# Optimization experiments

Measured on AMD Instinct MI355X. Metric: run time of the kernel, lower is better.

## Reference

```python
import jax, jax.numpy as jnp
import numpy as np

FRAMES, PATCHES, DIM, HEADS, DFF, K = 256, 64, 512, 8, 1024, 128


def _mhsa(x, Wqkv, Wo, h):
    # standard multi-head self-attention, no bias, no norm (as in the repo)
    b, t, d = x.shape
    dh = d // h
    qkv = x @ Wqkv                                   # [b, t, 3d]
    q, k, v = jnp.split(qkv, 3, axis=-1)
    rs = lambda z: z.reshape(b, t, h, dh).transpose(0, 2, 1, 3)  # [b,h,t,dh]
    q, k, v = rs(q), rs(k), rs(v)
    att = jax.nn.softmax(jnp.einsum('bhqd,bhkd->bhqk', q, k) * (dh ** -0.5), axis=-1)
    out = jnp.einsum('bhqk,bhkd->bhqd', att, v)
    return out.transpose(0, 2, 1, 3).reshape(b, t, d) @ Wo


def _linformer(x, Wqkv, Wo, E, h):
    # Linformer: project K and V along the token axis with E before attention
    b, t, d = x.shape
    dh = d // h
    qkv = x @ Wqkv
    q, k, v = jnp.split(qkv, 3, axis=-1)
    rs = lambda z: z.reshape(b, t, h, dh).transpose(0, 2, 1, 3)
    q, k, v = rs(q), rs(k), rs(v)
    k = jnp.einsum('bhjd,jk->bhkd', k, E)            # [b,h,K,dh]
    v = jnp.einsum('bhjd,jk->bhkd', v, E)
    att = jax.nn.softmax(jnp.einsum('bhqd,bhkd->bhqk', q, k) * (dh ** -0.5), axis=-1)
    out = jnp.einsum('bhqk,bhkd->bhqd', att, v)
    return out.transpose(0, 2, 1, 3).reshape(b, t, d) @ Wo


def setup_inputs() -> dict:
    key = jax.random.key(0)
    ks = jax.random.split(key, 10)
    s = 0.02
    n = 1 + FRAMES * PATCHES
    return {
        'x': jax.random.normal(ks[0], (1, n, DIM), jnp.float32),
        'Wqkv_t': jax.random.normal(ks[1], (DIM, 3 * DIM), jnp.float32) * s,
        'Wo_t': jax.random.normal(ks[2], (DIM, DIM), jnp.float32) * s,
        'Wqkv_s': jax.random.normal(ks[3], (DIM, 3 * DIM), jnp.float32) * s,
        'Wo_s': jax.random.normal(ks[4], (DIM, DIM), jnp.float32) * s,
        'E': jax.random.normal(ks[5], (PATCHES + 1, K), jnp.float32) * s,
        'W1': jax.random.normal(ks[6], (DIM, DFF), jnp.float32) * s,
        'b1': jnp.zeros((DFF,), jnp.float32),
        'W2': jax.random.normal(ks[7], (DFF, DIM), jnp.float32) * s,
        'b2': jnp.zeros((DIM,), jnp.float32),
    }


def reference(x, Wqkv_t, Wo_t, Wqkv_s, Wo_s, E, W1, b1, W2, b2):
    b, n, d = x.shape
    f, p = FRAMES, PATCHES
    # split cls token
    cls, xt = x[:, :1], x[:, 1:]                      # [b,1,d], [b,f*p,d]
    # rearrange 'b (f p) d -> (b p) f d'
    xt = xt.reshape(b, f, p, d).transpose(0, 2, 1, 3).reshape(b * p, f, d)
    cls_t = jnp.tile(cls, (b * p // b, 1, 1))          # expand cls to batch b*p
    xt = jnp.concatenate([cls_t, xt], axis=1)          # [b*p, f+1, d]
    y = _mhsa(xt, Wqkv_t, Wo_t, HEADS) + xt            # time attention + residual
    cls2, y = y[:, :1], y[:, 1:]                       # [b*p,1,d], [b*p,f,d]
    # rearrange '(b p) f d -> (b f) p d'
    y = y.reshape(b, p, f, d).transpose(0, 2, 1, 3).reshape(b * f, p, d)
    cls_s = jnp.tile(cls2, (b * f // (b * p), 1, 1))   # expand cls to batch b*f
    y = jnp.concatenate([cls_s, y], axis=1)            # [b*f, p+1, d]
    y = _linformer(y, Wqkv_s, Wo_s, E, HEADS) + y      # space attention + residual
    # rearrange '(b f) p d -> b (f p) d' (token count is p+1 here, per source)
    y = y.reshape(b, f * (p + 1), d)
    h = jax.nn.gelu(y @ W1 + b1, approximate=False)    # nn.GELU is exact erf
    y = (h @ W2 + b2) + y                              # MLP + residual (dropout=eval)
    return y
```

## Files before the change

### kernel.cpp

```cpp
#include <hip/hip_runtime.h>


typedef unsigned short u16;
typedef unsigned int   u32;
typedef __attribute__((ext_vector_type(8))) short s16x8;
typedef __attribute__((ext_vector_type(4))) float f32x4;

__device__ __forceinline__ float b2f(u16 u) {
    return __uint_as_float(((u32)u) << 16);
}
__device__ __forceinline__ u16 f2b(float f) {
    u32 v = __float_as_uint(f);
    return (u16)((v + 0x7FFFu + ((v >> 16) & 1u)) >> 16);
}

__global__ __launch_bounds__(128) void build_xt_k(const float* __restrict__ x,
                                                  u16* __restrict__ xt) {
    int row = blockIdx.x;
    int p = row / 257, t = row % 257;
    long src = (t == 0) ? 0L : (long)(1 + (t - 1) * 64 + p);
    float4 v = ((const float4*)(x + src * 512))[threadIdx.x];
    ushort4 o;
    o.x = f2b(v.x); o.y = f2b(v.y); o.z = f2b(v.z); o.w = f2b(v.w);
    ((ushort4*)(xt + (long)row * 512))[threadIdx.x] = o;
}

__global__ __launch_bounds__(128) void build_ys_k(const u16* __restrict__ yt,
                                                  u16* __restrict__ ys) {
    int row = blockIdx.x;
    int f = row / 65, s = row % 65;
    long src = (s == 0) ? (long)((f & 63) * 257) : (long)((s - 1) * 257 + 1 + f);
    const uint2* sp = (const uint2*)(yt + src * 512);
    ((uint2*)(ys + (long)row * 512))[threadIdx.x] = sp[threadIdx.x];
}

__global__ __launch_bounds__(256) void store_f32(const u16* __restrict__ src,
                                                 float* __restrict__ dst) {
    long i = ((long)blockIdx.x * 256 + threadIdx.x) * 8;
    uint4 v = *(const uint4*)(src + i);
    float4 a, b;
    a.x = b2f((u16)v.x); a.y = b2f((u16)(v.x >> 16));
    a.z = b2f((u16)v.y); a.w = b2f((u16)(v.y >> 16));
    b.x = b2f((u16)v.z); b.y = b2f((u16)(v.z >> 16));
    b.z = b2f((u16)v.w); b.w = b2f((u16)(v.w >> 16));
    *(float4*)(dst + i) = a;
    *(float4*)(dst + i + 4) = b;
}

__global__ __launch_bounds__(256) void prep_wt(const float* __restrict__ src,
                                               u16* __restrict__ dst,
                                               int K, int N) {
    __shared__ float T[64][65];
    int k0 = blockIdx.x * 64, n0 = blockIdx.y * 64;
    int t = threadIdx.x;
    int r = t >> 2, q = t & 3;
#pragma unroll
    for (int i = 0; i < 4; ++i) {
        float4 v = *(const float4*)(src + (long)(k0 + r) * N + n0 + q * 16 + i * 4);
        T[r][q * 16 + i * 4 + 0] = v.x;
        T[r][q * 16 + i * 4 + 1] = v.y;
        T[r][q * 16 + i * 4 + 2] = v.z;
        T[r][q * 16 + i * 4 + 3] = v.w;
    }
    __syncthreads();
    u32 buf[8];
#pragma unroll
    for (int i = 0; i < 8; ++i) {
        float lo = T[q * 16 + 2 * i][r];
        float hi = T[q * 16 + 2 * i + 1][r];
        buf[i] = (u32)f2b(lo) | ((u32)f2b(hi) << 16);
    }
    u32* dp = (u32*)(dst + (long)(n0 + r) * K + k0 + q * 16);
#pragma unroll
    for (int i = 0; i < 8; ++i) dp[i] = buf[i];
}

template <int EPI, int OD>
__global__ __launch_bounds__(256) void gemm_mt(const u16* __restrict__ A, int lda,
                                               const u16* __restrict__ WT, int ldwt,
                                               int koff, int coff,
                                               const float* __restrict__ bias, int coff_b,
                                               const u16* __restrict__ res,
                                               void* __restrict__ outv,
                                               int Kd, int ldo) {
    __shared__ __align__(16) u16 As2[4][64][8];
    __shared__ __align__(16) u16 Bs2[4][256][8];
    const int tid = threadIdx.x;
    const int lane = tid & 63, w = tid >> 6;
    const int l15 = lane & 15, kg = lane >> 4;
    const int bn0 = blockIdx.x * 256, bm0 = blockIdx.y * 64;

    f32x4 acc[4][4];
#pragma unroll
    for (int i = 0; i < 4; ++i)
#pragma unroll
        for (int j = 0; j < 4; ++j) acc[i][j] = (f32x4){0.f, 0.f, 0.f, 0.f};

    const u16* Abase = A + (long)(bm0 + (tid >> 2)) * lda + (tid & 3) * 8;
    const u16* Bbase = WT + (long)(coff + bn0 + (tid >> 2)) * ldwt + koff + (tid & 3) * 8;
    const long bstep = (long)64 * ldwt;

    uint4 av  = *(const uint4*)(Abase);
    uint4 bv0 = *(const uint4*)(Bbase);
    uint4 bv1 = *(const uint4*)(Bbase + bstep);
    uint4 bv2 = *(const uint4*)(Bbase + 2 * bstep);
    uint4 bv3 = *(const uint4*)(Bbase + 3 * bstep);

    for (int kt = 0; kt < Kd; kt += 32) {
        __syncthreads();
        *(uint4*)&As2[tid & 3][tid >> 2][0] = av;
        *(uint4*)&Bs2[tid & 3][(tid >> 2) + 0][0]   = bv0;
        *(uint4*)&Bs2[tid & 3][(tid >> 2) + 64][0]  = bv1;
        *(uint4*)&Bs2[tid & 3][(tid >> 2) + 128][0] = bv2;
        *(uint4*)&Bs2[tid & 3][(tid >> 2) + 192][0] = bv3;
        int ktn = (kt + 32 < Kd) ? (kt + 32) : kt;
        av  = *(const uint4*)(Abase + ktn);
        bv0 = *(const uint4*)(Bbase + ktn);
        bv1 = *(const uint4*)(Bbase + ktn + bstep);
        bv2 = *(const uint4*)(Bbase + ktn + 2 * bstep);
        bv3 = *(const uint4*)(Bbase + ktn + 3 * bstep);
        __syncthreads();
        s16x8 af[4], bfr[4];
#pragma unroll
        for (int mf = 0; mf < 4; ++mf)
            af[mf] = *(const s16x8*)&As2[kg][mf * 16 + l15][0];
#pragma unroll
        for (int nf = 0; nf < 4; ++nf)
            bfr[nf] = *(const s16x8*)&Bs2[kg][w * 64 + nf * 16 + l15][0];
#pragma unroll
        for (int mf = 0; mf < 4; ++mf)
#pragma unroll
            for (int nf = 0; nf < 4; ++nf)
                acc[mf][nf] = __builtin_amdgcn_mfma_f32_16x16x32_bf16(
                    af[mf], bfr[nf], acc[mf][nf], 0, 0, 0);
    }

#pragma unroll
    for (int mf = 0; mf < 4; ++mf) {
#pragma unroll
        for (int nf = 0; nf < 4; ++nf) {
            int col = bn0 + w * 64 + nf * 16 + l15;
#pragma unroll
            for (int r = 0; r < 4; ++r) {
                int row = bm0 + mf * 16 + kg * 4 + r;
                float v = acc[mf][nf][r];
                if (EPI == 2 || EPI == 3) v += bias[coff_b + col];
                if (EPI == 2) v = 0.5f * v * (1.f + erff(v * 0.70710678118f));
                if (EPI == 1 || EPI == 3) v += b2f(res[(long)row * ldo + col]);
                if (OD == 0) ((u16*)outv)[(long)row * ldo + col] = f2b(v);
                else         ((float*)outv)[(long)row * ldo + col] = v;
            }
        }
    }
}

template <int EPI, int OD>
__global__ __launch_bounds__(256) void gemm_k(const u16* __restrict__ A, int lda,
                                              const float* __restrict__ W, int ldw,
                                              int koff, int coff,
                                              const float* __restrict__ bias, int coff_b,
                                              const u16* __restrict__ res,
                                              void* __restrict__ outv,
                                              int M, int N, int Kd, int ldo) {
    __shared__ float As[16][64];
    __shared__ float Ws[16][128];
    int tid = threadIdx.x;
    int tx = tid & 15, ty = tid >> 4;
    int bn0 = blockIdx.x * 128, bm0 = blockIdx.y * 64;

    float acc[4][8];
#pragma unroll
    for (int i = 0; i < 4; ++i)
#pragma unroll
        for (int j = 0; j < 8; ++j) acc[i][j] = 0.f;

    int am = tid >> 2, ak = (tid & 3) * 4;
    int wk = tid >> 4, wn = (tid & 15) * 8;
    const u16* Aptr = A + (long)(bm0 + am) * lda + ak;

    for (int kt = 0; kt < Kd; kt += 16) {
        const u32* ap = (const u32*)(Aptr + kt);
        u32 a0 = ap[0], a1 = ap[1];
        const float* wp = W + (long)(koff + kt + wk) * ldw + coff + bn0 + wn;
        float4 w0 = ((const float4*)wp)[0];
        float4 w1 = ((const float4*)wp)[1];
        __syncthreads();
        As[ak + 0][am] = b2f((u16)a0);
        As[ak + 1][am] = b2f((u16)(a0 >> 16));
        As[ak + 2][am] = b2f((u16)a1);
        As[ak + 3][am] = b2f((u16)(a1 >> 16));
        Ws[wk][wn + 0] = w0.x; Ws[wk][wn + 1] = w0.y;
        Ws[wk][wn + 2] = w0.z; Ws[wk][wn + 3] = w0.w;
        Ws[wk][wn + 4] = w1.x; Ws[wk][wn + 5] = w1.y;
        Ws[wk][wn + 6] = w1.z; Ws[wk][wn + 7] = w1.w;
        __syncthreads();
#pragma unroll
        for (int kk = 0; kk < 16; ++kk) {
            float a[4], b[8];
#pragma unroll
            for (int i = 0; i < 4; ++i) a[i] = As[kk][ty + 16 * i];
#pragma unroll
            for (int j = 0; j < 8; ++j) b[j] = Ws[kk][tx + 16 * j];
#pragma unroll
            for (int i = 0; i < 4; ++i)
#pragma unroll
                for (int j = 0; j < 8; ++j) acc[i][j] += a[i] * b[j];
        }
    }

#pragma unroll
    for (int i = 0; i < 4; ++i) {
        int row = bm0 + ty + 16 * i;
#pragma unroll
        for (int j = 0; j < 8; ++j) {
            int col = bn0 + tx + 16 * j;
            float v = acc[i][j];
            if (EPI == 2 || EPI == 3) v += bias[coff_b + col];
            if (EPI == 2) v = 0.5f * v * (1.f + erff(v * 0.70710678118f));
            if (EPI == 1 || EPI == 3) v += b2f(res[(long)row * ldo + col]);
            if (OD == 0) ((u16*)outv)[(long)row * ldo + col] = f2b(v);
            else         ((float*)outv)[(long)row * ldo + col] = v;
        }
    }
}

__global__ __launch_bounds__(256) void attn_t3(u16* __restrict__ QO,
                                               const u16* __restrict__ Kg,
                                               const u16* __restrict__ Vg,
                                               int hbase, int qbase) {
    __shared__ __align__(16) u16 sm[17280];
    const int tid = threadIdx.x;
    const int lane = tid & 63, w = tid >> 6;
    const int l15 = lane & 15, kg = lane >> 4;
    const int seq = blockIdx.x >> 2, hq = blockIdx.x & 3, h = hbase + hq;
    const int qc = blockIdx.y;
    const long row0 = (long)seq * 257;
    const int qcol = qbase + hq * 64;
    const int rb = qc * 128 + w * 32;

    u16* Kb = sm;
    u16* Vb = sm + 4224;
    u16* Pw = sm + 8320 + w * 2240;

    const u32* Ku = (const u32*)Kg;
    const u32* Vu = (const u32*)Vg;

    s16x8 qf[2][2];
#pragma unroll
    for (int mf = 0; mf < 2; ++mf) {
        int row = rb + mf * 16 + l15;
#pragma unroll
        for (int ks = 0; ks < 2; ++ks) {
            if (row < 257)
                qf[mf][ks] = *(const s16x8*)(QO + (row0 + row) * 512 + qcol + ks * 32 + kg * 8);
            else
                qf[mf][ks] = (s16x8){0, 0, 0, 0, 0, 0, 0, 0};
        }
    }

    f32x4 acc_o[2][4];
    float m[2][4], l[2][4];
#pragma unroll
    for (int mf = 0; mf < 2; ++mf)
#pragma unroll
        for (int i = 0; i < 4; ++i) {
            acc_o[mf][i] = (f32x4){0.f, 0.f, 0.f, 0.f};
            m[mf][i] = -3.0e38f;
            l[mf][i] = 0.f;
        }

    for (int kc = 0; kc < 320; kc += 64) {
        __syncthreads();
        for (int idx = tid; idx < 2048; idx += 256) {
            int key = idx >> 5, cu = idx & 31, d0 = cu * 2;
            int kk = kc + key; if (kk > 256) kk = 256;
            u32 kv = Ku[(row0 + kk) * 256 + h * 32 + cu];
            *(u32*)&Kb[(((cu >> 2) * 66 + key) << 3) + (d0 & 7)] = kv;
        }
#pragma unroll
        for (int it = 0; it < 2; ++it) {
            int kg2 = (tid >> 6) + it * 4;
            int d = tid & 63;
            int sh = (d & 1) * 16;
            long vcol = hq * 32 + (d >> 1);
            u32 pk[4];
#pragma unroll
            for (int jp = 0; jp < 4; ++jp) {
                int k0 = kc + kg2 * 8 + 2 * jp;
                int k1 = k0 + 1;
                if (k0 > 256) k0 = 256;
                if (k1 > 256) k1 = 256;
                u32 a = Vu[(row0 + k0) * 128 + vcol];
                u32 b = Vu[(row0 + k1) * 128 + vcol];
                pk[jp] = ((a >> sh) & 0xFFFFu) | (((b >> sh) & 0xFFFFu) << 16);
            }
            uint4 vv; vv.x = pk[0]; vv.y = pk[1]; vv.z = pk[2]; vv.w = pk[3];
            *(uint4*)&Vb[(kg2 * 64 + d) << 3] = vv;
        }
        __syncthreads();

        s16x8 kbf[2][4];
#pragma unroll
        for (int ks = 0; ks < 2; ++ks)
#pragma unroll
            for (int nf = 0; nf < 4; ++nf)
                kbf[ks][nf] = *(const s16x8*)&Kb[(((ks * 4 + kg) * 66 + nf * 16 + l15) << 3)];

        const bool lastc = (kc == 256);
#pragma unroll
        for (int mf = 0; mf < 2; ++mf) {
            f32x4 accs[4];
#pragma unroll
            for (int nf = 0; nf < 4; ++nf) accs[nf] = (f32x4){0.f, 0.f, 0.f, 0.f};
#pragma unroll
            for (int ks = 0; ks < 2; ++ks)
#pragma unroll
                for (int nf = 0; nf < 4; ++nf)
                    accs[nf] = __builtin_amdgcn_mfma_f32_16x16x32_bf16(
                        qf[mf][ks], kbf[ks][nf], accs[nf], 0, 0, 0);
#pragma unroll
            for (int r = 0; r < 4; ++r) {
                float sv[4];
#pragma unroll
                for (int nf = 0; nf < 4; ++nf) sv[nf] = accs[nf][r] * 0.125f;
                if (lastc) {
#pragma unroll
                    for (int nf = 0; nf < 4; ++nf)
                        if (nf * 16 + l15 > 0) sv[nf] = -3.0e38f;
                }
                float mx = fmaxf(fmaxf(sv[0], sv[1]), fmaxf(sv[2], sv[3]));
                mx = fmaxf(mx, __shfl_xor(mx, 1));
                mx = fmaxf(mx, __shfl_xor(mx, 2));
                mx = fmaxf(mx, __shfl_xor(mx, 4));
                mx = fmaxf(mx, __shfl_xor(mx, 8));
                if (mx > m[mf][r] + 8.f) {
                    float sc = __expf(m[mf][r] - mx);
                    l[mf][r] *= sc;
#pragma unroll
                    for (int nf = 0; nf < 4; ++nf) acc_o[mf][nf][r] *= sc;
                    m[mf][r] = mx;
                }
                float pl = 0.f;
                u16 pb[4];
#pragma unroll
                for (int nf = 0; nf < 4; ++nf) {
                    float p = __expf(sv[nf] - m[mf][r]);
                    pl += p;
                    pb[nf] = f2b(p);
                }
                pl += __shfl_xor(pl, 1);
                pl += __shfl_xor(pl, 2);
                pl += __shfl_xor(pl, 4);
                pl += __shfl_xor(pl, 8);
                l[mf][r] += pl;
                const int rr = mf * 16 + kg * 4 + r;
#pragma unroll
                for (int nf = 0; nf < 4; ++nf)
                    Pw[(((nf * 2 + (l15 >> 3)) * 35 + rr) << 3) + (l15 & 7)] = pb[nf];
            }
        }
#pragma unroll
        for (int ks2 = 0; ks2 < 2; ++ks2) {
            s16x8 vbf[4];
#pragma unroll
            for (int nf = 0; nf < 4; ++nf)
                vbf[nf] = *(const s16x8*)&Vb[(((ks2 * 4 + kg) * 64 + nf * 16 + l15) << 3)];
#pragma unroll
            for (int mf = 0; mf < 2; ++mf) {
                s16x8 pa = *(const s16x8*)&Pw[(((ks2 * 4 + kg) * 35 + mf * 16 + l15) << 3)];
#pragma unroll
                for (int nf = 0; nf < 4; ++nf)
                    acc_o[mf][nf] = __builtin_amdgcn_mfma_f32_16x16x32_bf16(
                        pa, vbf[nf], acc_o[mf][nf], 0, 0, 0);
            }
        }
    }

#pragma unroll
    for (int mf = 0; mf < 2; ++mf) {
#pragma unroll
        for (int r = 0; r < 4; ++r) {
            int row = rb + mf * 16 + kg * 4 + r;
            if (row < 257) {
                float inv = 1.f / l[mf][r];
#pragma unroll
                for (int nf = 0; nf < 4; ++nf)
                    QO[(row0 + row) * 512 + qcol + nf * 16 + l15] =
                        f2b(acc_o[mf][nf][r] * inv);
            }
        }
    }
}

__global__ __launch_bounds__(320) void attn_t2(u16* __restrict__ QO,
                                               const u16* __restrict__ Kg,
                                               const u16* __restrict__ Vg,
                                               int hbase, int qbase_u32) {
    __shared__ u32 Ks[2080];
    __shared__ u32 Vs[2080];
    const int seq = blockIdx.x >> 2, hq = blockIdx.x & 3, h = hbase + hq;
    const int qc = blockIdx.y;
    const int tid = threadIdx.x;
    const int quad = tid >> 2, kq = tid & 3;
    const long row0 = (long)seq * 257;
    const int nq = (qc == 3) ? 65 : 64;
    const bool act = quad < nq;

    u32* QOu = (u32*)QO;
    const u32* Ku = (const u32*)Kg;
    const u32* Vu = (const u32*)Vg;

    const long qaddr = (row0 + qc * 64 + quad) * 256 + qbase_u32 + hq * 32 + kq * 8;

    float q[16], oacc[16];
#pragma unroll
    for (int i = 0; i < 16; ++i) { q[i] = 0.f; oacc[i] = 0.f; }
    if (act) {
        uint4 a = ((const uint4*)(QOu + qaddr))[0];
        uint4 b = ((const uint4*)(QOu + qaddr))[1];
        q[0]  = b2f((u16)a.x); q[1]  = b2f((u16)(a.x >> 16));
        q[2]  = b2f((u16)a.y); q[3]  = b2f((u16)(a.y >> 16));
        q[4]  = b2f((u16)a.z); q[5]  = b2f((u16)(a.z >> 16));
        q[6]  = b2f((u16)a.w); q[7]  = b2f((u16)(a.w >> 16));
        q[8]  = b2f((u16)b.x); q[9]  = b2f((u16)(b.x >> 16));
        q[10] = b2f((u16)b.y); q[11] = b2f((u16)(b.y >> 16));
        q[12] = b2f((u16)b.z); q[13] = b2f((u16)(b.z >> 16));
        q[14] = b2f((u16)b.w); q[15] = b2f((u16)(b.w >> 16));
    }
    float m = -3.0e38f, l = 0.f;

    for (int cc = 0; cc < 4; ++cc) {
        const int c0 = cc << 6;
        const int cn = (cc == 3) ? 65 : 64;
        __syncthreads();
        for (int idx = tid; idx < (cn << 5); idx += 320) {
            int r = idx >> 5, c = idx & 31;
            long grow = row0 + c0 + r;
            Ks[idx] = Ku[grow * 256 + h * 32 + c];
            Vs[idx] = Vu[grow * 128 + hq * 32 + c];
        }
        __syncthreads();
        if (act) {
            for (int j = 0; j < cn; ++j) {
                const uint4* kp = (const uint4*)(Ks + (j << 5) + (kq << 3));
                uint4 ka = kp[0], kb = kp[1];
                float s =
                    q[0]  * b2f((u16)ka.x) + q[1]  * b2f((u16)(ka.x >> 16)) +
                    q[2]  * b2f((u16)ka.y) + q[3]  * b2f((u16)(ka.y >> 16)) +
                    q[4]  * b2f((u16)ka.z) + q[5]  * b2f((u16)(ka.z >> 16)) +
                    q[6]  * b2f((u16)ka.w) + q[7]  * b2f((u16)(ka.w >> 16)) +
                    q[8]  * b2f((u16)kb.x) + q[9]  * b2f((u16)(kb.x >> 16)) +
                    q[10] * b2f((u16)kb.y) + q[11] * b2f((u16)(kb.y >> 16)) +
                    q[12] * b2f((u16)kb.z) + q[13] * b2f((u16)(kb.z >> 16)) +
                    q[14] * b2f((u16)kb.w) + q[15] * b2f((u16)(kb.w >> 16));
                s += __shfl_xor(s, 1);
                s += __shfl_xor(s, 2);
                s *= 0.125f;
                if (s > m + 8.f) {
                    float sc = __expf(m - s);
                    l *= sc;
#pragma unroll
                    for (int i = 0; i < 16; ++i) oacc[i] *= sc;
                    m = s;
                }
                float p = __expf(s - m);
                l += p;
                const uint4* vp = (const uint4*)(Vs + (j << 5) + (kq << 3));
                uint4 va = vp[0], vb = vp[1];
                oacc[0]  += p * b2f((u16)va.x); oacc[1]  += p * b2f((u16)(va.x >> 16));
                oacc[2]  += p * b2f((u16)va.y); oacc[3]  += p * b2f((u16)(va.y >> 16));
                oacc[4]  += p * b2f((u16)va.z); oacc[5]  += p * b2f((u16)(va.z >> 16));
                oacc[6]  += p * b2f((u16)va.w); oacc[7]  += p * b2f((u16)(va.w >> 16));
                oacc[8]  += p * b2f((u16)vb.x); oacc[9]  += p * b2f((u16)(vb.x >> 16));
                oacc[10] += p * b2f((u16)vb.y); oacc[11] += p * b2f((u16)(vb.y >> 16));
                oacc[12] += p * b2f((u16)vb.z); oacc[13] += p * b2f((u16)(vb.z >> 16));
                oacc[14] += p * b2f((u16)vb.w); oacc[15] += p * b2f((u16)(vb.w >> 16));
            }
        }
    }
    if (act) {
        float inv = 1.f / l;
        uint4 o0, o1;
        o0.x = (u32)f2b(oacc[0]  * inv) | ((u32)f2b(oacc[1]  * inv) << 16);
        o0.y = (u32)f2b(oacc[2]  * inv) | ((u32)f2b(oacc[3]  * inv) << 16);
        o0.z = (u32)f2b(oacc[4]  * inv) | ((u32)f2b(oacc[5]  * inv) << 16);
        o0.w = (u32)f2b(oacc[6]  * inv) | ((u32)f2b(oacc[7]  * inv) << 16);
        o1.x = (u32)f2b(oacc[8]  * inv) | ((u32)f2b(oacc[9]  * inv) << 16);
        o1.y = (u32)f2b(oacc[10] * inv) | ((u32)f2b(oacc[11] * inv) << 16);
        o1.z = (u32)f2b(oacc[12] * inv) | ((u32)f2b(oacc[13] * inv) << 16);
        o1.w = (u32)f2b(oacc[14] * inv) | ((u32)f2b(oacc[15] * inv) << 16);
        ((uint4*)(QOu + qaddr))[0] = o0;
        ((uint4*)(QOu + qaddr))[1] = o1;
    }
}

__global__ __launch_bounds__(320) void attn_s2(const u16* __restrict__ Qg,
                                               const u16* __restrict__ Kg,
                                               u16* __restrict__ Vg,
                                               const float* __restrict__ E,
                                               int hbase) {
    __shared__ u32 smu[14882];
    u32* Kpt = smu;
    u32* Es2 = smu + 4352;
    u32* Ks2 = smu + 8512;
    u32* Vs2 = smu + 10592;
    u32* Qs2 = smu + 12672;

    const int bid = blockIdx.x, f = bid >> 2, hq = bid & 3, h = hbase + hq;
    const int tid = threadIdx.x;
    const long rbase = (long)f * 65;
    const u32* Kgu = (const u32*)Kg;
    u32* Vgu = (u32*)Vg;
    const u32* Qgu = (const u32*)Qg;

    for (int idx = tid; idx < 4160; idx += 320) {
        float e0 = E[2 * idx], e1 = E[2 * idx + 1];
        Es2[idx] = (u32)f2b(e0) | ((u32)f2b(e1) << 16);
    }
    for (int idx = tid; idx < 2080; idx += 320) {
        int r = idx >> 5, c = idx & 31;
        long src = (rbase + r) * 256 + h * 32 + c;
        Ks2[r * 32 + c] = Kgu[src];
        Vs2[r * 32 + c] = Vgu[src];
        Qs2[r * 34 + c] = Qgu[(rbase + r) * 128 + hq * 32 + c];
    }
    __syncthreads();

    if (tid < 256) {
        const int d = tid >> 2, kq4 = tid & 3;
        float kp[32];
#pragma unroll
        for (int i = 0; i < 32; ++i) kp[i] = 0.f;
        const u16* Ku = (const u16*)Ks2;
        for (int j = 0; j < 65; ++j) {
            float kv = b2f(Ku[j * 64 + d]);
            const uint4* ep = (const uint4*)(Es2 + j * 64 + kq4 * 16);
#pragma unroll
            for (int i4 = 0; i4 < 4; ++i4) {
                uint4 e4 = ep[i4];
                kp[i4 * 8 + 0] += kv * b2f((u16)e4.x);
                kp[i4 * 8 + 1] += kv * b2f((u16)(e4.x >> 16));
                kp[i4 * 8 + 2] += kv * b2f((u16)e4.y);
                kp[i4 * 8 + 3] += kv * b2f((u16)(e4.y >> 16));
                kp[i4 * 8 + 4] += kv * b2f((u16)e4.z);
                kp[i4 * 8 + 5] += kv * b2f((u16)(e4.z >> 16));
                kp[i4 * 8 + 6] += kv * b2f((u16)e4.w);
                kp[i4 * 8 + 7] += kv * b2f((u16)(e4.w >> 16));
            }
        }
        u32* ko = Kpt + d * 68 + kq4 * 16;
#pragma unroll
        for (int i2 = 0; i2 < 16; ++i2)
            ko[i2] = (u32)f2b(kp[2 * i2]) | ((u32)f2b(kp[2 * i2 + 1]) << 16);
    }
    __syncthreads();

    const int q = tid >> 2, kq = tid & 3;
    if (q < 65) {
        float s[32];
#pragma unroll
        for (int i = 0; i < 32; ++i) s[i] = 0.f;
        const u32* qrow = Qs2 + q * 34;
        for (int d2 = 0; d2 < 32; ++d2) {
            u32 qw = qrow[d2];
            float q0 = b2f((u16)qw), q1 = b2f((u16)(qw >> 16));
            const uint4* r0 = (const uint4*)(Kpt + (2 * d2) * 68 + kq * 16);
            const uint4* r1 = (const uint4*)(Kpt + (2 * d2 + 1) * 68 + kq * 16);
#pragma unroll
            for (int i4 = 0; i4 < 4; ++i4) {
                uint4 a = r0[i4], b = r1[i4];
                s[i4 * 8 + 0] += q0 * b2f((u16)a.x) + q1 * b2f((u16)b.x);
                s[i4 * 8 + 1] += q0 * b2f((u16)(a.x >> 16)) + q1 * b2f((u16)(b.x >> 16));
                s[i4 * 8 + 2] += q0 * b2f((u16)a.y) + q1 * b2f((u16)b.y);
                s[i4 * 8 + 3] += q0 * b2f((u16)(a.y >> 16)) + q1 * b2f((u16)(b.y >> 16));
                s[i4 * 8 + 4] += q0 * b2f((u16)a.z) + q1 * b2f((u16)b.z);
                s[i4 * 8 + 5] += q0 * b2f((u16)(a.z >> 16)) + q1 * b2f((u16)(b.z >> 16));
                s[i4 * 8 + 6] += q0 * b2f((u16)a.w) + q1 * b2f((u16)b.w);
                s[i4 * 8 + 7] += q0 * b2f((u16)(a.w >> 16)) + q1 * b2f((u16)(b.w >> 16));
            }
        }
        float m = -3.0e38f;
#pragma unroll
        for (int i = 0; i < 32; ++i) { s[i] *= 0.125f; m = fmaxf(m, s[i]); }
        m = fmaxf(m, __shfl_xor(m, 1));
        m = fmaxf(m, __shfl_xor(m, 2));
        float l = 0.f;
#pragma unroll
        for (int i = 0; i < 32; ++i) { s[i] = __expf(s[i] - m); l += s[i]; }
        l += __shfl_xor(l, 1);
        l += __shfl_xor(l, 2);

        float o[16];
#pragma unroll
        for (int i = 0; i < 16; ++i) o[i] = 0.f;
        for (int j = 0; j < 65; ++j) {
            const uint4* ep = (const uint4*)(Es2 + j * 64 + kq * 16);
            float pe = 0.f;
#pragma unroll
            for (int i4 = 0; i4 < 4; ++i4) {
                uint4 e4 = ep[i4];
                pe += s[i4 * 8 + 0] * b2f((u16)e4.x) + s[i4 * 8 + 1] * b2f((u16)(e4.x >> 16))
                    + s[i4 * 8 + 2] * b2f((u16)e4.y) + s[i4 * 8 + 3] * b2f((u16)(e4.y >> 16))
                    + s[i4 * 8 + 4] * b2f((u16)e4.z) + s[i4 * 8 + 5] * b2f((u16)(e4.z >> 16))
                    + s[i4 * 8 + 6] * b2f((u16)e4.w) + s[i4 * 8 + 7] * b2f((u16)(e4.w >> 16));
            }
            pe += __shfl_xor(pe, 1);
            pe += __shfl_xor(pe, 2);
            const uint4* vp = (const uint4*)(Vs2 + j * 32 + kq * 8);
#pragma unroll
            for (int i4 = 0; i4 < 2; ++i4) {
                uint4 v4 = vp[i4];
                o[i4 * 8 + 0] += pe * b2f((u16)v4.x);
                o[i4 * 8 + 1] += pe * b2f((u16)(v4.x >> 16));
                o[i4 * 8 + 2] += pe * b2f((u16)v4.y);
                o[i4 * 8 + 3] += pe * b2f((u16)(v4.y >> 16));
                o[i4 * 8 + 4] += pe * b2f((u16)v4.z);
                o[i4 * 8 + 5] += pe * b2f((u16)(v4.z >> 16));
                o[i4 * 8 + 6] += pe * b2f((u16)v4.w);
                o[i4 * 8 + 7] += pe * b2f((u16)(v4.w >> 16));
            }
        }
        float inv = 1.f / l;
        u32* op = Vgu + (rbase + q) * 256 + h * 32 + kq * 8;
#pragma unroll
        for (int i = 0; i < 8; ++i)
            op[i] = (u32)f2b(o[2 * i] * inv) | ((u32)f2b(o[2 * i + 1] * inv) << 16);
    }
}

__global__ __launch_bounds__(256) void attn_s3(const u16* __restrict__ Qg,
                                               const u16* __restrict__ Kg,
                                               u16* __restrict__ Vg,
                                               const float* __restrict__ E,
                                               int hbase) {
    __shared__ __align__(16) u16 sm[33024];
    u16* ET8 = sm;
    u16* KT8 = sm + 8192;
    u16* VT8 = sm + 12288;
    u16* Er  = sm + 16384;
    u16* Kr  = sm + 16512;
    u16* Vr  = sm + 16576;
    u16* Q8  = sm;
    u16* P16 = sm + 5120;
    float* Srow = (float*)(sm + 15360);
    u16* Kp8   = sm + 16640;
    u16* VpT16 = sm + 24832;

    const int bid = blockIdx.x, f = bid >> 2, hq = bid & 3, h = hbase + hq;
    const int tid = threadIdx.x;
    const int lane = tid & 63, w = tid >> 6;
    const int l15 = lane & 15, kg = lane >> 4;
    const long rbase = (long)f * 65;
    const u32* Kgu = (const u32*)Kg;
    u32* Vgu = (u32*)Vg;
    const u32* Qgu = (const u32*)Qg;

    for (int idx = tid; idx < 8320; idx += 256) {
        int j = idx >> 7, kL = idx & 127;
        u16 v = f2b(E[idx]);
        if (j < 64) ET8[(((j >> 3) * 128 + kL) << 3) + (j & 7)] = v;
        else        Er[kL] = v;
    }
    for (int idx = tid; idx < 2080; idx += 256) {
        int j = idx >> 5, cu = idx & 31;
        long src = (rbase + j) * 256 + h * 32 + cu;
        u32 kv = Kgu[src], vv = Vgu[src];
        int d0 = cu * 2;
        if (j < 64) {
            int base = (j >> 3), jj = j & 7;
            KT8[(((base) * 64 + d0) << 3) + jj]     = (u16)kv;
            KT8[(((base) * 64 + d0 + 1) << 3) + jj] = (u16)(kv >> 16);
            VT8[(((base) * 64 + d0) << 3) + jj]     = (u16)vv;
            VT8[(((base) * 64 + d0 + 1) << 3) + jj] = (u16)(vv >> 16);
        } else {
            Kr[d0] = (u16)kv; Kr[d0 + 1] = (u16)(kv >> 16);
            Vr[d0] = (u16)vv; Vr[d0 + 1] = (u16)(vv >> 16);
        }
    }
    __syncthreads();

    {
        f32x4 acc[2][4];
#pragma unroll
        for (int i = 0; i < 2; ++i)
#pragma unroll
            for (int j2 = 0; j2 < 4; ++j2) acc[i][j2] = (f32x4){0.f, 0.f, 0.f, 0.f};
#pragma unroll
        for (int ks = 0; ks < 2; ++ks) {
            int c = ks * 4 + kg;
            s16x8 a0 = *(const s16x8*)&ET8[((c * 128 + (2 * w) * 16 + l15) << 3)];
            s16x8 a1 = *(const s16x8*)&ET8[((c * 128 + (2 * w + 1) * 16 + l15) << 3)];
            s16x8 b0 = *(const s16x8*)&KT8[((c * 64 + 0 * 16 + l15) << 3)];
            s16x8 b1 = *(const s16x8*)&KT8[((c * 64 + 1 * 16 + l15) << 3)];
            s16x8 b2v = *(const s16x8*)&KT8[((c * 64 + 2 * 16 + l15) << 3)];
            s16x8 b3 = *(const s16x8*)&KT8[((c * 64 + 3 * 16 + l15) << 3)];
            acc[0][0] = __builtin_amdgcn_mfma_f32_16x16x32_bf16(a0, b0, acc[0][0], 0, 0, 0);
            acc[0][1] = __builtin_amdgcn_mfma_f32_16x16x32_bf16(a0, b1, acc[0][1], 0, 0, 0);
            acc[0][2] = __builtin_amdgcn_mfma_f32_16x16x32_bf16(a0, b2v, acc[0][2], 0, 0, 0);
            acc[0][3] = __builtin_amdgcn_mfma_f32_16x16x32_bf16(a0, b3, acc[0][3], 0, 0, 0);
            acc[1][0] = __builtin_amdgcn_mfma_f32_16x16x32_bf16(a1, b0, acc[1][0], 0, 0, 0);
            acc[1][1] = __builtin_amdgcn_mfma_f32_16x16x32_bf16(a1, b1, acc[1][1], 0, 0, 0);
            acc[1][2] = __builtin_amdgcn_mfma_f32_16x16x32_bf16(a1, b2v, acc[1][2], 0, 0, 0);
            acc[1][3] = __builtin_amdgcn_mfma_f32_16x16x32_bf16(a1, b3, acc[1][3], 0, 0, 0);
        }
#pragma unroll
        for (int mi = 0; mi < 2; ++mi)
#pragma unroll
            for (int nf = 0; nf < 4; ++nf) {
                int d = nf * 16 + l15;
                float kr = b2f(Kr[d]);
                int cidx = (nf * 2 + (l15 >> 3));
#pragma unroll
                for (int r = 0; r < 4; ++r) {
                    int kL = (2 * w + mi) * 16 + kg * 4 + r;
                    float v = acc[mi][nf][r] + b2f(Er[kL]) * kr;
                    Kp8[((cidx * 128 + kL) << 3) + (l15 & 7)] = f2b(v);
                }
            }
    }

    {
        f32x4 acc[8];
#pragma unroll
        for (int i = 0; i < 8; ++i) acc[i] = (f32x4){0.f, 0.f, 0.f, 0.f};
#pragma unroll
        for (int ks = 0; ks < 2; ++ks) {
            int c = ks * 4 + kg;
            s16x8 a = *(const s16x8*)&VT8[((c * 64 + w * 16 + l15) << 3)];
#pragma unroll
            for (int nf = 0; nf < 8; ++nf) {
                s16x8 b = *(const s16x8*)&ET8[((c * 128 + nf * 16 + l15) << 3)];
                acc[nf] = __builtin_amdgcn_mfma_f32_16x16x32_bf16(a, b, acc[nf], 0, 0, 0);
            }
        }
#pragma unroll
        for (int nf = 0; nf < 8; ++nf) {
            int kL = nf * 16 + l15;
            float er = b2f(Er[kL]);
            int cidx = (nf * 2 + (l15 >> 3));
#pragma unroll
            for (int r = 0; r < 4; ++r) {
                int d = w * 16 + kg * 4 + r;
                float v = acc[nf][r] + b2f(Vr[d]) * er;
                VpT16[((cidx * 64 + d) << 3) + (l15 & 7)] = f2b(v);
            }
        }
    }
    __syncthreads();

    for (int idx = tid; idx < 2560; idx += 256) {
        int rq = idx >> 5, cu = idx & 31;
        u32 val = (rq < 65) ? Qgu[(rbase + rq) * 128 + hq * 32 + cu] : 0u;
        *(u32*)&Q8[(((cu >> 2) * 80 + rq) << 3) + ((2 * cu) & 7)] = val;
    }
    __syncthreads();

    {
        f32x4 accs[8], acc4[2];
#pragma unroll
        for (int i = 0; i < 8; ++i) accs[i] = (f32x4){0.f, 0.f, 0.f, 0.f};
#pragma unroll
        for (int i = 0; i < 2; ++i) acc4[i] = (f32x4){0.f, 0.f, 0.f, 0.f};
#pragma unroll
        for (int ks = 0; ks < 2; ++ks) {
            int c = ks * 4 + kg;
            s16x8 a = *(const s16x8*)&Q8[((c * 80 + w * 16 + l15) << 3)];
            s16x8 a4 = *(const s16x8*)&Q8[((c * 80 + 64 + l15) << 3)];
#pragma unroll
            for (int nf = 0; nf < 8; ++nf) {
                s16x8 b = *(const s16x8*)&Kp8[((c * 128 + nf * 16 + l15) << 3)];
                accs[nf] = __builtin_amdgcn_mfma_f32_16x16x32_bf16(a, b, accs[nf], 0, 0, 0);
            }
#pragma unroll
            for (int i = 0; i < 2; ++i) {
                int nf4 = 2 * w + i;
                s16x8 b = *(const s16x8*)&Kp8[((c * 128 + nf4 * 16 + l15) << 3)];
                acc4[i] = __builtin_amdgcn_mfma_f32_16x16x32_bf16(a4, b, acc4[i], 0, 0, 0);
            }
        }
#pragma unroll
        for (int r = 0; r < 4; ++r) {
            float sv[8];
            float mx = -3.0e38f;
#pragma unroll
            for (int nf = 0; nf < 8; ++nf) {
                sv[nf] = accs[nf][r] * 0.125f;
                mx = fmaxf(mx, sv[nf]);
            }
            mx = fmaxf(mx, __shfl_xor(mx, 1));
            mx = fmaxf(mx, __shfl_xor(mx, 2));
            mx = fmaxf(mx, __shfl_xor(mx, 4));
            mx = fmaxf(mx, __shfl_xor(mx, 8));
            float l = 0.f;
#pragma unroll
            for (int nf = 0; nf < 8; ++nf) { sv[nf] = __expf(sv[nf] - mx); l += sv[nf]; }
            l += __shfl_xor(l, 1);
            l += __shfl_xor(l, 2);
            l += __shfl_xor(l, 4);
            l += __shfl_xor(l, 8);
            float inv = 1.f / l;
            int row = w * 16 + kg * 4 + r;
#pragma unroll
            for (int nf = 0; nf < 8; ++nf)
                P16[(((nf * 2 + (l15 >> 3)) * 80 + row) << 3) + (l15 & 7)] = f2b(sv[nf] * inv);
        }
        if (kg == 0) {
#pragma unroll
            for (int i = 0; i < 2; ++i)
                Srow[(2 * w + i) * 16 + l15] = acc4[i][0] * 0.125f;
        }
        for (int idx = tid; idx < 1920; idx += 256) {
            int row = 65 + (idx >> 7), col = idx & 127;
            P16[(((col >> 3) * 80 + row) << 3) + (col & 7)] = 0;
        }
    }
    __syncthreads();

    if (w == 0) {
        float v0 = Srow[lane], v1 = Srow[lane + 64];
        float mx = fmaxf(v0, v1);
#pragma unroll
        for (int s = 1; s < 64; s <<= 1) mx = fmaxf(mx, __shfl_xor(mx, s));
        float p0 = __expf(v0 - mx), p1 = __expf(v1 - mx);
        float l = p0 + p1;
#pragma unroll
        for (int s = 1; s < 64; s <<= 1) l += __shfl_xor(l, s);
        float inv = 1.f / l;
        int c0 = lane, c1 = lane + 64;
        P16[(((c0 >> 3) * 80 + 64) << 3) + (c0 & 7)] = f2b(p0 * inv);
        P16[(((c1 >> 3) * 80 + 64) << 3) + (c1 & 7)] = f2b(p1 * inv);
    }
    __syncthreads();

    {
        f32x4 acco[4], acco4;
#pragma unroll
        for (int i = 0; i < 4; ++i) acco[i] = (f32x4){0.f, 0.f, 0.f, 0.f};
        acco4 = (f32x4){0.f, 0.f, 0.f, 0.f};
#pragma unroll
        for (int ks = 0; ks < 4; ++ks) {
            int c = ks * 4 + kg;
            s16x8 a = *(const s16x8*)&P16[((c * 80 + w * 16 + l15) << 3)];
            s16x8 a4 = *(const s16x8*)&P16[((c * 80 + 64 + l15) << 3)];
#pragma unroll
            for (int nf = 0; nf < 4; ++nf) {
                s16x8 b = *(const s16x8*)&VpT16[((c * 64 + nf * 16 + l15) << 3)];
                acco[nf] = __builtin_amdgcn_mfma_f32_16x16x32_bf16(a, b, acco[nf], 0, 0, 0);
            }
            s16x8 b4 = *(const s16x8*)&VpT16[((c * 64 + w * 16 + l15) << 3)];
            acco4 = __builtin_amdgcn_mfma_f32_16x16x32_bf16(a4, b4, acco4, 0, 0, 0);
        }
        u16* Vg16 = (u16*)Vgu;
#pragma unroll
        for (int nf = 0; nf < 4; ++nf) {
            int d = nf * 16 + l15;
#pragma unroll
            for (int r = 0; r < 4; ++r) {
                int q = w * 16 + kg * 4 + r;
                Vg16[(rbase + q) * 512 + h * 64 + d] = f2b(acco[nf][r]);
            }
        }
        if (kg == 0) {
            int d = w * 16 + l15;
            Vg16[(rbase + 64) * 512 + h * 64 + d] = f2b(acco4[0]);
        }
    }
}

extern "C" void kernel_launch(void* const* d_in, const int* in_sizes, int n_in,
                              void* d_out, int out_size, void* d_ws, size_t ws_size,
                              hipStream_t stream) {
    int ix = 0, iE = 5, ib1 = 7, ib2 = 9;
    int q1 = -1, q2 = -1, o1 = -1, o2 = -1, w1 = -1, w2 = -1;
    for (int i = 0; i < n_in; ++i) {
        int s = in_sizes[i];
        if (s == 8389120) { if (ix != i && i == 0) ix = i; else if (in_sizes[ix] != 8389120) ix = i; }
        else if (s == 8320) iE = i;
        else if (s == 1024) ib1 = i;
        else if (s == 512) ib2 = i;
        else if (s == 786432) { if (q1 < 0) q1 = i; else q2 = i; }
        else if (s == 262144) { if (o1 < 0) o1 = i; else o2 = i; }
        else if (s == 524288) { if (w1 < 0) w1 = i; else w2 = i; }
    }
    if (q1 < 0) q1 = 1; if (o1 < 0) o1 = 2;
    if (q2 < 0) q2 = 3; if (o2 < 0) o2 = 4;
    if (w1 < 0) w1 = 6; if (ib1 < 0) ib1 = 7;
    if (w2 < 0) w2 = 8;

    const float* x      = (const float*)d_in[ix];
    const float* Wqkv_t = (const float*)d_in[q1];
    const float* Wo_t   = (const float*)d_in[o1];
    const float* Wqkv_s = (const float*)d_in[q2];
    const float* Wo_s   = (const float*)d_in[o2];
    const float* E      = (const float*)d_in[iE];
    const float* W1     = (const float*)d_in[w1];
    const float* b1     = (const float*)d_in[ib1];
    const float* W2     = (const float*)d_in[w2];
    const float* b2     = (const float*)d_in[ib2];

    float* outf = (float*)d_out;
    u16* D0 = (u16*)d_out;
    u16* B = (u16*)d_ws;
    u16* H = B + 8519680L;
    u16* D0up = D0 + 8519680L;

    const bool mfma = (ws_size >= 31850496UL);

    if (mfma) {
        u16* WT1 = H + 4259840L;
        u16* WT2 = WT1 + 786432L;
        u16* WT3 = WT2 + 262144L;
        u16* WT4 = WT3 + 786432L;
        u16* WT5 = WT4 + 262144L;
        u16* WT6 = WT5 + 524288L;

        prep_wt<<<dim3(8, 24), 256, 0, stream>>>(Wqkv_t, WT1, 512, 1536);
        prep_wt<<<dim3(8, 8),  256, 0, stream>>>(Wo_t,   WT2, 512, 512);
        prep_wt<<<dim3(8, 24), 256, 0, stream>>>(Wqkv_s, WT3, 512, 1536);
        prep_wt<<<dim3(8, 8),  256, 0, stream>>>(Wo_s,   WT4, 512, 512);
        prep_wt<<<dim3(8, 16), 256, 0, stream>>>(W1,     WT5, 512, 1024);
        prep_wt<<<dim3(16, 8), 256, 0, stream>>>(W2,     WT6, 1024, 512);

        build_xt_k<<<16448, 128, 0, stream>>>(x, B);
        gemm_mt<0, 0><<<dim3(2, 257), 256, 0, stream>>>(B, 512, WT1, 512, 0, 512,
                                                        nullptr, 0, nullptr, D0up, 512, 512);
        gemm_mt<0, 0><<<dim3(2, 257), 256, 0, stream>>>(B, 512, WT1, 512, 0, 0,
                                                        nullptr, 0, nullptr, D0, 512, 512);
        gemm_mt<0, 0><<<dim3(1, 257), 256, 0, stream>>>(B, 512, WT1, 512, 0, 1024,
                                                        nullptr, 0, nullptr, H, 512, 256);
        attn_t3<<<dim3(256, 3), 256, 0, stream>>>(D0, D0up, H, 0, 0);
        gemm_mt<0, 0><<<dim3(1, 257), 256, 0, stream>>>(B, 512, WT1, 512, 0, 1280,
                                                        nullptr, 0, nullptr, H, 512, 256);
        attn_t3<<<dim3(256, 3), 256, 0, stream>>>(D0, D0up, H, 4, 256);
        gemm_mt<1, 0><<<dim3(2, 257), 256, 0, stream>>>(D0, 512, WT2, 512, 0, 0,
                                                        nullptr, 0, B, B, 512, 512);
        build_ys_k<<<16640, 128, 0, stream>>>(B, D0);
        gemm_mt<0, 0><<<dim3(2, 260), 256, 0, stream>>>(D0, 512, WT3, 512, 0, 512,
                                                        nullptr, 0, nullptr, B, 512, 512);
        gemm_mt<0, 0><<<dim3(2, 260), 256, 0, stream>>>(D0, 512, WT3, 512, 0, 1024,
                                                        nullptr, 0, nullptr, D0up, 512, 512);
        gemm_mt<0, 0><<<dim3(1, 260), 256, 0, stream>>>(D0, 512, WT3, 512, 0, 0,
                                                        nullptr, 0, nullptr, H, 512, 256);
        attn_s3<<<1024, 256, 0, stream>>>(H, B, D0up, E, 0);
        gemm_mt<0, 0><<<dim3(1, 260), 256, 0, stream>>>(D0, 512, WT3, 512, 0, 256,
                                                        nullptr, 0, nullptr, H, 512, 256);
        attn_s3<<<1024, 256, 0, stream>>>(H, B, D0up, E, 4);
        gemm_mt<1, 0><<<dim3(2, 260), 256, 0, stream>>>(D0up, 512, WT4, 512, 0, 0,
                                                        nullptr, 0, D0, D0, 512, 512);
        gemm_mt<2, 0><<<dim3(2, 260), 256, 0, stream>>>(D0, 512, WT5, 512, 0, 0,
                                                        b1, 0, nullptr, D0up, 512, 512);
        gemm_mt<3, 0><<<dim3(2, 260), 256, 0, stream>>>(D0up, 512, WT6, 1024, 0, 0,
                                                        b2, 0, D0, B, 512, 512);
        gemm_mt<2, 0><<<dim3(2, 260), 256, 0, stream>>>(D0, 512, WT5, 512, 0, 512,
                                                        b1, 512, nullptr, D0up, 512, 512);
        gemm_mt<1, 0><<<dim3(2, 260), 256, 0, stream>>>(D0up, 512, WT6, 1024, 512, 0,
                                                        nullptr, 0, B, B, 512, 512);
        store_f32<<<4160, 256, 0, stream>>>(B, outf);
    } else {
        build_xt_k<<<16448, 128, 0, stream>>>(x, B);
        gemm_k<0, 0><<<dim3(4, 257), 256, 0, stream>>>(B, 512, Wqkv_t, 1536, 0, 512,
                                                       nullptr, 0, nullptr, D0up,
                                                       16448, 512, 512, 512);
        gemm_k<0, 0><<<dim3(2, 257), 256, 0, stream>>>(B, 512, Wqkv_t, 1536, 0, 1024,
                                                       nullptr, 0, nullptr, H,
                                                       16448, 256, 512, 256);
        gemm_k<0, 0><<<dim3(2, 257), 256, 0, stream>>>(B, 512, Wqkv_t, 1536, 0, 0,
                                                       nullptr, 0, nullptr, D0,
                                                       16448, 256, 512, 512);
        attn_t2<<<dim3(256, 4), 320, 0, stream>>>(D0, D0up, H, 0, 0);
        gemm_k<0, 0><<<dim3(2, 257), 256, 0, stream>>>(B, 512, Wqkv_t, 1536, 0, 1280,
                                                       nullptr, 0, nullptr, H,
                                                       16448, 256, 512, 256);
        gemm_k<0, 0><<<dim3(2, 257), 256, 0, stream>>>(B, 512, Wqkv_t, 1536, 0, 256,
                                                       nullptr, 0, nullptr, D0 + 256,
                                                       16448, 256, 512, 512);
        attn_t2<<<dim3(256, 4), 320, 0, stream>>>(D0, D0up, H, 4, 128);
        gemm_k<1, 0><<<dim3(4, 257), 256, 0, stream>>>(D0, 512, Wo_t, 512, 0, 0,
                                                       nullptr, 0, B, B,
                                                       16448, 512, 512, 512);
        build_ys_k<<<16640, 128, 0, stream>>>(B, D0);
        gemm_k<0, 0><<<dim3(4, 260), 256, 0, stream>>>(D0, 512, Wqkv_s, 1536, 0, 512,
                                                       nullptr, 0, nullptr, B,
                                                       16640, 512, 512, 512);
        gemm_k<0, 0><<<dim3(4, 260), 256, 0, stream>>>(D0, 512, Wqkv_s, 1536, 0, 1024,
                                                       nullptr, 0, nullptr, D0up,
                                                       16640, 512, 512, 512);
        gemm_k<0, 0><<<dim3(2, 260), 256, 0, stream>>>(D0, 512, Wqkv_s, 1536, 0, 0,
                                                       nullptr, 0, nullptr, H,
                                                       16640, 256, 512, 256);
        attn_s2<<<1024, 320, 0, stream>>>(H, B, D0up, E, 0);
        gemm_k<0, 0><<<dim3(2, 260), 256, 0, stream>>>(D0, 512, Wqkv_s, 1536, 0, 256,
                                                       nullptr, 0, nullptr, H,
                                                       16640, 256, 512, 256);
        attn_s2<<<1024, 320, 0, stream>>>(H, B, D0up, E, 4);
        gemm_k<1, 0><<<dim3(4, 260), 256, 0, stream>>>(D0up, 512, Wo_s, 512, 0, 0,
                                                       nullptr, 0, D0, D0,
                                                       16640, 512, 512, 512);
        for (int qd = 0; qd < 4; ++qd) {
            gemm_k<2, 0><<<dim3(2, 260), 256, 0, stream>>>(D0, 512, W1, 1024, 0, qd * 256,
                                                           b1, qd * 256, nullptr, H,
                                                           16640, 256, 512, 256);
            if (qd == 0)
                gemm_k<3, 0><<<dim3(4, 260), 256, 0, stream>>>(H, 256, W2, 512, qd * 256, 0,
                                                               b2, 0, D0, B,
                                                               16640, 512, 256, 512);
            else if (qd < 3)
                gemm_k<1, 0><<<dim3(4, 260), 256, 0, stream>>>(H, 256, W2, 512, qd * 256, 0,
                                                               nullptr, 0, B, B,
                                                               16640, 512, 256, 512);
            else
                gemm_k<1, 1><<<dim3(4, 260), 256, 0, stream>>>(H, 256, W2, 512, qd * 256, 0,
                                                               nullptr, 0, B, outf,
                                                               16640, 512, 256, 512);
        }
    }
}
```

Measured before the change: 680.5 us.

## Use direct global-to-LDS loads with double buffering and XOR swizzle in GEMM

The GEMM main loop now loads A and B tiles straight into LDS with global_load_lds instead of staging through registers. It uses two LDS buffers so the next K-tile streams in while MFMAs run on the current one, which removes one barrier per iteration. It also switches to a row-major [row][32] layout with an XOR swizzle to avoid bank conflicts on fragment reads. The cost is double the LDS footprint and a reliance on correct ordering of the asynchronous LDS writes against a single barrier.

```diff
diff --git a/kernel.cpp b/kernel.cpp
--- a/kernel.cpp
+++ b/kernel.cpp
@@ -12,6 +12,12 @@
 __device__ __forceinline__ u16 f2b(float f) {
     u32 v = __float_as_uint(f);
     return (u16)((v + 0x7FFFu + ((v >> 16) & 1u)) >> 16);
+}
+
+__device__ __forceinline__ void gload16(const u16* g, u16* l) {
+    __builtin_amdgcn_global_load_lds(
+        (const __attribute__((address_space(1))) u32*)(const void*)g,
+        (__attribute__((address_space(3))) u32*)(void*)l, 16, 0, 0);
 }
 
 __global__ __launch_bounds__(128) void build_xt_k(const float* __restrict__ x,
@@ -83,8 +89,8 @@
                                                const u16* __restrict__ res,
                                                void* __restrict__ outv,
                                                int Kd, int ldo) {
-    __shared__ __align__(16) u16 As2[4][64][8];
-    __shared__ __align__(16) u16 Bs2[4][256][8];
+    __shared__ __align__(16) u16 As3[2][64][32];
+    __shared__ __align__(16) u16 Bs3[2][256][32];
     const int tid = threadIdx.x;
     const int lane = tid & 63, w = tid >> 6;
     const int l15 = lane & 15, kg = lane >> 4;
@@ -96,43 +102,52 @@
 #pragma unroll
         for (int j = 0; j < 4; ++j) acc[i][j] = (f32x4){0.f, 0.f, 0.f, 0.f};
 
-    const u16* Abase = A + (long)(bm0 + (tid >> 2)) * lda + (tid & 3) * 8;
-    const u16* Bbase = WT + (long)(coff + bn0 + (tid >> 2)) * ldwt + koff + (tid & 3) * 8;
-    const long bstep = (long)64 * ldwt;
-
-    uint4 av  = *(const uint4*)(Abase);
-    uint4 bv0 = *(const uint4*)(Bbase);
-    uint4 bv1 = *(const uint4*)(Bbase + bstep);
-    uint4 bv2 = *(const uint4*)(Bbase + 2 * bstep);
-    uint4 bv3 = *(const uint4*)(Bbase + 3 * bstep);
-
+    const int srow = w * 16 + (lane >> 2);
+    const int sga  = (lane & 3) ^ ((srow >> 1) & 3);
+    const u16* gA = A + (long)(bm0 + srow) * lda + sga * 8;
+    const u16* gB[4];
+#pragma unroll
+    for (int i = 0; i < 4; ++i) {
+        int scol = w * 64 + i * 16 + (lane >> 2);
+        int sgb = (lane & 3) ^ ((scol >> 1) & 3);
+        gB[i] = WT + (long)(coff + bn0 + scol) * ldwt + koff + sgb * 8;
+    }
+
+    gload16(gA, &As3[0][w * 16][0]);
+#pragma unroll
+    for (int i = 0; i < 4; ++i)
+        gload16(gB[i], &Bs3[0][w * 64 + i * 16][0]);
+    __syncthreads();
+
+    int cur = 0;
     for (int kt = 0; kt < Kd; kt += 32) {
-        __syncthreads();
-        *(uint4*)&As2[tid & 3][tid >> 2][0] = av;
-        *(uint4*)&Bs2[tid & 3][(tid >> 2) + 0][0]   = bv0;
-        *(uint4*)&Bs2[tid & 3][(tid >> 2) + 64][0]  = bv1;
-        *(uint4*)&Bs2[tid & 3][(tid >> 2) + 128][0] = bv2;
-        *(uint4*)&Bs2[tid & 3][(tid >> 2) + 192][0] = bv3;
-        int ktn = (kt + 32 < Kd) ? (kt + 32) : kt;
-        av  = *(const uint4*)(Abase + ktn);
-        bv0 = *(const uint4*)(Bbase + ktn);
-        bv1 = *(const uint4*)(Bbase + ktn + bstep);
-        bv2 = *(const uint4*)(Bbase + ktn + 2 * bstep);
-        bv3 = *(const uint4*)(Bbase + ktn + 3 * bstep);
-        __syncthreads();
+        if (kt + 32 < Kd) {
+            gload16(gA + kt + 32, &As3[cur ^ 1][w * 16][0]);
+#pragma unroll
+            for (int i = 0; i < 4; ++i)
+                gload16(gB[i] + kt + 32, &Bs3[cur ^ 1][w * 64 + i * 16][0]);
+        }
         s16x8 af[4], bfr[4];
 #pragma unroll
-        for (int mf = 0; mf < 4; ++mf)
-            af[mf] = *(const s16x8*)&As2[kg][mf * 16 + l15][0];
-#pragma unroll
-        for (int nf = 0; nf < 4; ++nf)
-            bfr[nf] = *(const s16x8*)&Bs2[kg][w * 64 + nf * 16 + l15][0];
+        for (int mf = 0; mf < 4; ++mf) {
+            int row = mf * 16 + l15;
+            int slot = kg ^ ((row >> 1) & 3);
+            af[mf] = *(const s16x8*)&As3[cur][row][slot * 8];
+        }
+#pragma unroll
+        for (int nf = 0; nf < 4; ++nf) {
+            int col = w * 64 + nf * 16 + l15;
+            int slot = kg ^ ((col >> 1) & 3);
+            bfr[nf] = *(const s16x8*)&Bs3[cur][col][slot * 8];
+        }
 #pragma unroll
         for (int mf = 0; mf < 4; ++mf)
 #pragma unroll
             for (int nf = 0; nf < 4; ++nf)
                 acc[mf][nf] = __builtin_amdgcn_mfma_f32_16x16x32_bf16(
                     af[mf], bfr[nf], acc[mf][nf], 0, 0, 0);
+        __syncthreads();
+        cur ^= 1;
     }
 
 #pragma unroll
```

After: 637.2 us. -6.4%, faster.
